# Kernel tuning notes

Measured on AMD Instinct MI355X. Metric: run time of the kernel, lower is better.

## Reference

```python
import jax, jax.numpy as jnp
import numpy as np

N_NODES = 50000
N_EDGES = 800000
IN_CH = 128
HID = 64
HEADS = 2
OUT_CH = 3
N_GRAPHS = 64
NEG_SLOPE = 0.2


def _gatv2(x, src, dst, Wl, Wr, att, bias, heads, out_ch, concat, n_nodes):
    # GATv2Conv (PyG semantics, eval mode, self-loops already appended)
    xl = (x @ Wl).reshape(n_nodes, heads, out_ch)  # lin_l -> source messages
    xr = (x @ Wr).reshape(n_nodes, heads, out_ch)  # lin_r -> target side
    e = jax.nn.leaky_relu(xl[src] + xr[dst], NEG_SLOPE)          # [E, H, C]
    alpha = jnp.einsum('ehc,hc->eh', e, att)                     # [E, H]
    # segment softmax over incoming edges of each target node
    amax = jax.ops.segment_max(alpha, dst, num_segments=n_nodes)  # [N, H]
    ea = jnp.exp(alpha - amax[dst])
    denom = jax.ops.segment_sum(ea, dst, num_segments=n_nodes)
    alpha = ea / (denom[dst] + 1e-16)
    msg = xl[src] * alpha[..., None]                             # [E, H, C]
    out = jax.ops.segment_sum(msg, dst, num_segments=n_nodes)    # [N, H, C]
    out = out.reshape(n_nodes, heads * out_ch) if concat else out.mean(axis=1)
    return out + bias


def setup_inputs() -> dict:
    key = jax.random.key(0)
    ks = jax.random.split(key, 12)
    x = jax.random.normal(ks[0], (N_NODES, IN_CH), dtype=jnp.float32)
    edge_index = jax.random.randint(ks[1], (2, N_EDGES), 0, N_NODES, dtype=jnp.int64 if jax.config.jax_enable_x64 else jnp.int32)
    batch = jnp.sort(jax.random.randint(ks[2], (N_NODES,), 0, N_GRAPHS))
    s = 0.05
    params = {
        'W1l': jax.random.normal(ks[3], (IN_CH, HEADS * HID), dtype=jnp.float32) * s,
        'W1r': jax.random.normal(ks[4], (IN_CH, HEADS * HID), dtype=jnp.float32) * s,
        'att1': jax.random.normal(ks[5], (HEADS, HID), dtype=jnp.float32) * s,
        'b1': jnp.zeros((HEADS * HID,), dtype=jnp.float32),
        'W2l': jax.random.normal(ks[6], (HEADS * HID, OUT_CH), dtype=jnp.float32) * s,
        'W2r': jax.random.normal(ks[7], (HEADS * HID, OUT_CH), dtype=jnp.float32) * s,
        'att2': jax.random.normal(ks[8], (1, OUT_CH), dtype=jnp.float32) * s,
        'b2': jnp.zeros((OUT_CH,), dtype=jnp.float32),
        'Wr1': jax.random.normal(ks[9], (OUT_CH, 64), dtype=jnp.float32) * s,
        'br1': jnp.zeros((64,), dtype=jnp.float32),
        'Wr2': jax.random.normal(ks[10], (64, 3), dtype=jnp.float32) * s,
        'br2': jnp.zeros((3,), dtype=jnp.float32),
    }
    return {'x': x, 'edge_index': edge_index, 'batch': batch, **params}


def reference(x, edge_index, batch, W1l, W1r, att1, b1, W2l, W2r, att2, b2, Wr1, br1, Wr2, br2):
    n = x.shape[0]
    loops = jnp.arange(n, dtype=edge_index.dtype)
    src = jnp.concatenate([edge_index[0], loops])  # add_self_loops=True
    dst = jnp.concatenate([edge_index[1], loops])
    h = _gatv2(x, src, dst, W1l, W1r, att1, b1, HEADS, HID, True, n)
    h = jax.nn.elu(h)
    h = _gatv2(h, src, dst, W2l, W2r, att2, b2, 1, OUT_CH, False, n)
    # global_mean_pool over graphs
    sums = jax.ops.segment_sum(h, batch, num_segments=N_GRAPHS)
    cnt = jax.ops.segment_sum(jnp.ones((n,), h.dtype), batch, num_segments=N_GRAPHS)
    g = sums / jnp.maximum(cnt, 1.0)[:, None]
    g = jax.nn.relu(g @ Wr1 + br1)
    return g @ Wr2 + br2
```

## Files before the change

### kernel.cpp

```cpp
#include <hip/hip_runtime.h>


#define NGRAPH 64
#define LOG2E 1.4426950408889634f

#define DPP_ROR(C, x) \
  __int_as_float(__builtin_amdgcn_update_dpp(0, __float_as_int(x), (0x120 | C), 0xF, 0xF, false))

__device__ __forceinline__ float rowsum16(float v) {
  v += DPP_ROR(8, v);
  v += DPP_ROR(4, v);
  v += DPP_ROR(2, v);
  v += DPP_ROR(1, v);
  return v;
}

__device__ __forceinline__ unsigned bf16rne(float f) {
  unsigned u = __float_as_uint(f);
  return (u + 0x7FFFu + ((u >> 16) & 1u)) >> 16;
}

__global__ void k_deg(const int* __restrict__ ei, int E, int Et,
                      int* __restrict__ deg, int* __restrict__ rank) {
  int e = blockIdx.x * blockDim.x + threadIdx.x;
  if (e >= Et) return;
  int d = (e < E) ? ei[E + e] : (e - E);
  rank[e] = atomicAdd(&deg[d], 1);
}

__global__ __launch_bounds__(256) void k_scan_part(const int* __restrict__ deg,
                                                   int* __restrict__ bsum, int n) {
  __shared__ int sd[256];
  int t = threadIdx.x;
  int i = blockIdx.x * 1024 + t * 4;
  int s = 0;
  if (i + 4 <= n) {
    int4 d = *(const int4*)&deg[i];
    s = d.x + d.y + d.z + d.w;
  } else {
    for (int j = i; j < min(i + 4, n); ++j) s += deg[j];
  }
  sd[t] = s;
  __syncthreads();
  for (int off = 128; off; off >>= 1) {
    if (t < off) sd[t] += sd[t + off];
    __syncthreads();
  }
  if (t == 0) bsum[blockIdx.x] = sd[0];
}

__global__ __launch_bounds__(64) void k_scan_top(int* __restrict__ bsum, int nb) {
  __shared__ int s[64];
  int t = threadIdx.x;
  s[t] = (t < nb) ? bsum[t] : 0;
  __syncthreads();
  int acc = 0;
  for (int j = 0; j < t; ++j) acc += s[j];
  if (t < nb) bsum[t] = acc;
}

__global__ __launch_bounds__(256) void k_scan_write(const int* __restrict__ deg,
                                                    const int* __restrict__ bsum,
                                                    int* __restrict__ row_ptr, int n) {
  __shared__ int sd[256];
  int t = threadIdx.x;
  int i = blockIdx.x * 1024 + t * 4;
  int4 d = make_int4(0, 0, 0, 0);
  bool full = (i + 4 <= n);
  if (full) d = *(const int4*)&deg[i];
  else {
    if (i + 0 < n) d.x = deg[i + 0];
    if (i + 1 < n) d.y = deg[i + 1];
    if (i + 2 < n) d.z = deg[i + 2];
    if (i + 3 < n) d.w = deg[i + 3];
  }
  int s = d.x + d.y + d.z + d.w;
  sd[t] = s;
  __syncthreads();
  for (int off = 1; off < 256; off <<= 1) {
    int v = (t >= off) ? sd[t - off] : 0;
    __syncthreads();
    sd[t] += v;
    __syncthreads();
  }
  int ex = sd[t] - s + bsum[blockIdx.x];
  int4 r;
  r.x = ex;
  r.y = ex + d.x;
  r.z = r.y + d.y;
  r.w = r.z + d.z;
  if (full) {
    *(int4*)&row_ptr[i] = r;
    if (i + 4 == n) row_ptr[n] = r.w + d.w;
  } else if (i < n) {
    int run = ex;
    int vals[4] = {d.x, d.y, d.z, d.w};
    for (int j = 0; j < 4 && i + j < n; ++j) {
      row_ptr[i + j] = run;
      run += vals[j];
    }
    if (i <= n && i + 4 > n) row_ptr[n] = run;
  }
}

__global__ void k_fill(const int* __restrict__ ei, int E, int Et,
                       const int* __restrict__ row_ptr,
                       const int* __restrict__ rank,
                       int* __restrict__ csr_src) {
  int e = blockIdx.x * blockDim.x + threadIdx.x;
  if (e >= Et) return;
  int s, d;
  if (e < E) { s = ei[e]; d = ei[E + e]; }
  else       { s = e - E; d = s; }
  csr_src[row_ptr[d] + rank[e]] = s;
}

__global__ __launch_bounds__(256) void k_gemm128(const float* __restrict__ x,
                                                 const float* __restrict__ Wl,
                                                 const float* __restrict__ Wr,
                                                 unsigned short* __restrict__ outl,
                                                 float* __restrict__ outr, int n) {
  __shared__ __align__(16) float xs[16][68];
  __shared__ __align__(16) float wsl[16][132];
  __shared__ __align__(16) float wsr[16][132];
  int t = threadIdx.x;
  int tx = t & 15, ty = t >> 4;
  int r0 = blockIdx.x * 64;
  float accl[4][8] = {};
  float accr[4][8] = {};

  int sr = t >> 2;
  int sk = (t & 3) * 4;
  int wk = t >> 5;
  int wc = (t & 31) * 4;

  for (int k0 = 0; k0 < 128; k0 += 16) {
    int gr = r0 + sr;
    float4 xv = make_float4(0.f, 0.f, 0.f, 0.f);
    if (gr < n) xv = *(const float4*)&x[(size_t)gr * 128 + k0 + sk];
    float4 wl0 = *(const float4*)&Wl[(size_t)(k0 + wk) * 128 + wc];
    float4 wl1 = *(const float4*)&Wl[(size_t)(k0 + wk + 8) * 128 + wc];
    float4 wr0 = *(const float4*)&Wr[(size_t)(k0 + wk) * 128 + wc];
    float4 wr1 = *(const float4*)&Wr[(size_t)(k0 + wk + 8) * 128 + wc];
    __syncthreads();
    xs[sk + 0][sr] = xv.x;
    xs[sk + 1][sr] = xv.y;
    xs[sk + 2][sr] = xv.z;
    xs[sk + 3][sr] = xv.w;
    *(float4*)&wsl[wk][wc] = wl0;
    *(float4*)&wsl[wk + 8][wc] = wl1;
    *(float4*)&wsr[wk][wc] = wr0;
    *(float4*)&wsr[wk + 8][wc] = wr1;
    __syncthreads();
#pragma unroll
    for (int k = 0; k < 16; ++k) {
      float4 av = *(const float4*)&xs[k][ty * 4];
      float4 bl0 = *(const float4*)&wsl[k][tx * 4];
      float4 bl1 = *(const float4*)&wsl[k][64 + tx * 4];
      float4 br0 = *(const float4*)&wsr[k][tx * 4];
      float4 br1 = *(const float4*)&wsr[k][64 + tx * 4];
      float a[4] = {av.x, av.y, av.z, av.w};
      float bl[8] = {bl0.x, bl0.y, bl0.z, bl0.w, bl1.x, bl1.y, bl1.z, bl1.w};
      float br[8] = {br0.x, br0.y, br0.z, br0.w, br1.x, br1.y, br1.z, br1.w};
#pragma unroll
      for (int i = 0; i < 4; ++i)
#pragma unroll
        for (int j = 0; j < 8; ++j) {
          accl[i][j] = fmaf(a[i], bl[j], accl[i][j]);
          accr[i][j] = fmaf(a[i], br[j], accr[i][j]);
        }
    }
  }
#pragma unroll
  for (int i = 0; i < 4; ++i) {
    int gr = r0 + ty * 4 + i;
    if (gr < n) {
      uint2 p0, p1;
      p0.x = bf16rne(accl[i][0]) | (bf16rne(accl[i][1]) << 16);
      p0.y = bf16rne(accl[i][2]) | (bf16rne(accl[i][3]) << 16);
      p1.x = bf16rne(accl[i][4]) | (bf16rne(accl[i][5]) << 16);
      p1.y = bf16rne(accl[i][6]) | (bf16rne(accl[i][7]) << 16);
      *(uint2*)&outl[(size_t)gr * 128 + tx * 4] = p0;
      *(uint2*)&outl[(size_t)gr * 128 + 64 + tx * 4] = p1;
      *(float4*)&outr[(size_t)gr * 128 + tx * 4] =
          make_float4(accr[i][0], accr[i][1], accr[i][2], accr[i][3]);
      *(float4*)&outr[(size_t)gr * 128 + 64 + tx * 4] =
          make_float4(accr[i][4], accr[i][5], accr[i][6], accr[i][7]);
    }
  }
}

__global__ __launch_bounds__(256) void k_fused1(const unsigned short* __restrict__ xl,
                                                const float* __restrict__ xr,
                                                const int* __restrict__ row_ptr,
                                                const int* __restrict__ csr_src,
                                                const float* __restrict__ att1,
                                                const float* __restrict__ b1,
                                                const float* __restrict__ W2l,
                                                const float* __restrict__ W2r,
                                                float* __restrict__ xl2,
                                                float* __restrict__ xr2, int n) {
  int wid  = (blockIdx.x * 256 + threadIdx.x) >> 6;
  int lane = threadIdx.x & 63;
  int sub  = lane & 31;
  int node = min(wid * 2 + (lane >> 5), n - 1);
  int ch = sub * 4;
  const char* xlb = (const char*)xl;
  unsigned chb = (unsigned)sub * 8u;
  float4 xrv = *(const float4*)&xr[(size_t)node * 128 + ch];
  float4 atv = *(const float4*)&att1[ch];
  atv.x *= LOG2E; atv.y *= LOG2E; atv.z *= LOG2E; atv.w *= LOG2E;
  int s0 = row_ptr[node];
  int deg = row_ptr[node + 1] - s0;
  int odeg = __shfl_xor(deg, 32);
  int mindeg = min(deg, odeg);
  int maxdeg = max(deg, odeg);
  const int* sp = csr_src + s0;

  float m = -1e30f, l = 0.f;
  float4 acc = make_float4(0.f, 0.f, 0.f, 0.f);

  float t0, t1, t2, t3;
#define UNPACK(dst, q)                                                  \
    dst.x = __uint_as_float(q.x << 16);                                 \
    dst.y = __uint_as_float(q.x & 0xFFFF0000u);                         \
    dst.z = __uint_as_float(q.y << 16);                                 \
    dst.w = __uint_as_float(q.y & 0xFFFF0000u);
#define LOGIT(p, v)                                                     \
    t0 = v.x + xrv.x; t0 = fmaxf(t0, 0.2f * t0);                        \
    t1 = v.y + xrv.y; t1 = fmaxf(t1, 0.2f * t1);                        \
    t2 = v.z + xrv.z; t2 = fmaxf(t2, 0.2f * t2);                        \
    t3 = v.w + xrv.w; t3 = fmaxf(t3, 0.2f * t3);                        \
    p = fmaf(t3, atv.w, fmaf(t2, atv.z, fmaf(t1, atv.y, t0 * atv.x)));

#define BODY(CLAMPED)                                                   \
  {                                                                     \
    int sA, sB, sC, sD;                                                 \
    if (CLAMPED) {                                                      \
      int dm1 = deg - 1;                                                \
      sA = sp[min(e + 0, dm1)];                                         \
      sB = sp[min(e + 1, dm1)];                                         \
      sC = sp[min(e + 2, dm1)];                                         \
      sD = sp[min(e + 3, dm1)];                                         \
    } else {                                                            \
      sA = sp[e + 0]; sB = sp[e + 1]; sC = sp[e + 2]; sD = sp[e + 3];   \
    }                                                                   \
    uint2 qa = *(const uint2*)(xlb + (((unsigned)sA << 8) + chb));      \
    uint2 qb = *(const uint2*)(xlb + (((unsigned)sB << 8) + chb));      \
    uint2 qc = *(const uint2*)(xlb + (((unsigned)sC << 8) + chb));      \
    uint2 qd = *(const uint2*)(xlb + (((unsigned)sD << 8) + chb));      \
    float4 xa, xb, xc, xd;                                              \
    UNPACK(xa, qa) UNPACK(xb, qb) UNPACK(xc, qc) UNPACK(xd, qd)         \
    float pa, pb, pc, pd;                                               \
    LOGIT(pa, xa) LOGIT(pb, xb) LOGIT(pc, xc) LOGIT(pd, xd)             \
    pa = rowsum16(pa);                                                  \
    pb = rowsum16(pb);                                                  \
    pc = rowsum16(pc);                                                  \
    pd = rowsum16(pd);                                                  \
    if (CLAMPED) {                                                      \
      pa = (e + 0 < deg) ? pa : -1e30f;                                 \
      pb = (e + 1 < deg) ? pb : -1e30f;                                 \
      pc = (e + 2 < deg) ? pc : -1e30f;                                 \
      pd = (e + 3 < deg) ? pd : -1e30f;                                 \
    }                                                                   \
    float mn = fmaxf(m, fmaxf(fmaxf(pa, pb), fmaxf(pc, pd)));           \
    float sc = exp2f(m - mn);                                           \
    float wa = exp2f(pa - mn);                                          \
    float wb = exp2f(pb - mn);                                          \
    float wc = exp2f(pc - mn);                                          \
    float wd = exp2f(pd - mn);                                          \
    acc.x = fmaf(wd, xd.x, fmaf(wc, xc.x, fmaf(wb, xb.x, fmaf(wa, xa.x, acc.x * sc)))); \
    acc.y = fmaf(wd, xd.y, fmaf(wc, xc.y, fmaf(wb, xb.y, fmaf(wa, xa.y, acc.y * sc)))); \
    acc.z = fmaf(wd, xd.z, fmaf(wc, xc.z, fmaf(wb, xb.z, fmaf(wa, xa.z, acc.z * sc)))); \
    acc.w = fmaf(wd, xd.w, fmaf(wc, xc.w, fmaf(wb, xb.w, fmaf(wa, xa.w, acc.w * sc)))); \
    l = fmaf(l, sc, wa + wb + wc + wd);                                 \
    m = mn;                                                             \
  }

  int e = 0;
  for (; e + 4 <= mindeg; e += 4) BODY(false)
  for (; e < maxdeg; e += 4) BODY(true)
#undef BODY
#undef LOGIT
#undef UNPACK

  float inv = 1.f / (l + 1e-16f);
  float4 b1v = *(const float4*)&b1[ch];
  float4 h;
  h.x = acc.x * inv + b1v.x; h.x = h.x > 0.f ? h.x : expm1f(h.x);
  h.y = acc.y * inv + b1v.y; h.y = h.y > 0.f ? h.y : expm1f(h.y);
  h.z = acc.z * inv + b1v.z; h.z = h.z > 0.f ? h.z : expm1f(h.z);
  h.w = acc.w * inv + b1v.w; h.w = h.w > 0.f ? h.w : expm1f(h.w);

  float4 u0 = *(const float4*)&W2l[ch * 3 + 0];
  float4 u1 = *(const float4*)&W2l[ch * 3 + 4];
  float4 u2 = *(const float4*)&W2l[ch * 3 + 8];
  float al0 = fmaf(h.w, u2.y, fmaf(h.z, u1.z, fmaf(h.y, u0.w, h.x * u0.x)));
  float al1 = fmaf(h.w, u2.z, fmaf(h.z, u1.w, fmaf(h.y, u1.x, h.x * u0.y)));
  float al2 = fmaf(h.w, u2.w, fmaf(h.z, u2.x, fmaf(h.y, u1.y, h.x * u0.z)));
  float4 v0 = *(const float4*)&W2r[ch * 3 + 0];
  float4 v1 = *(const float4*)&W2r[ch * 3 + 4];
  float4 v2 = *(const float4*)&W2r[ch * 3 + 8];
  float ar0 = fmaf(h.w, v2.y, fmaf(h.z, v1.z, fmaf(h.y, v0.w, h.x * v0.x)));
  float ar1 = fmaf(h.w, v2.z, fmaf(h.z, v1.w, fmaf(h.y, v1.x, h.x * v0.y)));
  float ar2 = fmaf(h.w, v2.w, fmaf(h.z, v2.x, fmaf(h.y, v1.y, h.x * v0.z)));
#pragma unroll
  for (int off = 1; off < 32; off <<= 1) {
    al0 += __shfl_xor(al0, off); al1 += __shfl_xor(al1, off);
    al2 += __shfl_xor(al2, off); ar0 += __shfl_xor(ar0, off);
    ar1 += __shfl_xor(ar1, off); ar2 += __shfl_xor(ar2, off);
  }
  if (sub == 0 && wid * 2 + (lane >> 5) < n) {
    *(float4*)&xl2[node * 4] = make_float4(al0, al1, al2, 0.f);
    *(float4*)&xr2[node * 4] = make_float4(ar0, ar1, ar2, 0.f);
  }
}

__global__ __launch_bounds__(256) void k_fused2(const float* __restrict__ xl2,
                                                const float* __restrict__ xr2,
                                                const int* __restrict__ row_ptr,
                                                const int* __restrict__ csr_src,
                                                const float* __restrict__ att2,
                                                const float* __restrict__ b2,
                                                const int* __restrict__ batch,
                                                float* __restrict__ gsum,
                                                float* __restrict__ gcnt, int n) {
  __shared__ float ls[NGRAPH * 3];
  __shared__ float lc[NGRAPH];
  int t = threadIdx.x;
  for (int i = t; i < NGRAPH * 3; i += 256) ls[i] = 0.f;
  for (int i = t; i < NGRAPH; i += 256) lc[i] = 0.f;
  __syncthreads();

  int node = (blockIdx.x * 256 + t) >> 4;
  int lane = t & 15;
  if (node < n) {
    float4 xrv = *(const float4*)&xr2[node * 4];
    float c0 = att2[0] * LOG2E, c1 = att2[1] * LOG2E, c2 = att2[2] * LOG2E;
    int s0 = row_ptr[node], s1 = row_ptr[node + 1];
    float m = -1e30f, l = 0.f, a0 = 0.f, a1 = 0.f, a2 = 0.f;
    for (int slot = s0 + lane; slot < s1; slot += 16) {
      int s = csr_src[slot];
      float4 xlv = *(const float4*)&xl2[s * 4];
      float t0 = xlv.x + xrv.x; t0 = fmaxf(t0, 0.2f * t0);
      float t1 = xlv.y + xrv.y; t1 = fmaxf(t1, 0.2f * t1);
      float t2 = xlv.z + xrv.z; t2 = fmaxf(t2, 0.2f * t2);
      float p = fmaf(t2, c2, fmaf(t1, c1, t0 * c0));
      float mn = fmaxf(m, p);
      float sc = exp2f(m - mn);
      float w  = exp2f(p - mn);
      a0 = a0 * sc + w * xlv.x;
      a1 = a1 * sc + w * xlv.y;
      a2 = a2 * sc + w * xlv.z;
      l = l * sc + w;
      m = mn;
    }
#define MERGE(C)                                                        \
    {                                                                   \
      float m2 = DPP_ROR(C, m);                                         \
      float l2 = DPP_ROR(C, l);                                         \
      float b0 = DPP_ROR(C, a0);                                        \
      float b1v = DPP_ROR(C, a1);                                       \
      float b2v = DPP_ROR(C, a2);                                       \
      float mn = fmaxf(m, m2);                                          \
      float sA = exp2f(m - mn);                                         \
      float sB = exp2f(m2 - mn);                                        \
      a0 = a0 * sA + b0 * sB;                                           \
      a1 = a1 * sA + b1v * sB;                                          \
      a2 = a2 * sA + b2v * sB;                                          \
      l = l * sA + l2 * sB;                                             \
      m = mn;                                                           \
    }
    MERGE(8) MERGE(4) MERGE(2) MERGE(1)
#undef MERGE
    if (lane == 0) {
      float inv = 1.f / (l + 1e-16f);
      float o0 = a0 * inv + b2[0];
      float o1 = a1 * inv + b2[1];
      float o2 = a2 * inv + b2[2];
      int b = batch[node];
      atomicAdd(&ls[b * 3 + 0], o0);
      atomicAdd(&ls[b * 3 + 1], o1);
      atomicAdd(&ls[b * 3 + 2], o2);
      atomicAdd(&lc[b], 1.f);
    }
  }
  __syncthreads();
  for (int i = t; i < NGRAPH * 3; i += 256)
    if (ls[i] != 0.f) atomicAdd(&gsum[i], ls[i]);
  for (int i = t; i < NGRAPH; i += 256)
    if (lc[i] != 0.f) atomicAdd(&gcnt[i], lc[i]);
}

__global__ __launch_bounds__(64) void k_mlp(const float* __restrict__ gsum,
                                            const float* __restrict__ gcnt,
                                            const float* __restrict__ Wr1,
                                            const float* __restrict__ br1,
                                            const float* __restrict__ Wr2,
                                            const float* __restrict__ br2,
                                            float* __restrict__ out) {
  int t = threadIdx.x;
  if (t >= NGRAPH) return;
  float cnt = fmaxf(gcnt[t], 1.f);
  float g0 = gsum[t * 3 + 0] / cnt;
  float g1 = gsum[t * 3 + 1] / cnt;
  float g2 = gsum[t * 3 + 2] / cnt;
  float o0 = br2[0], o1 = br2[1], o2 = br2[2];
  for (int j = 0; j < 64; ++j) {
    float hj = g0 * Wr1[j] + g1 * Wr1[64 + j] + g2 * Wr1[128 + j] + br1[j];
    hj = fmaxf(hj, 0.f);
    o0 = fmaf(hj, Wr2[j * 3 + 0], o0);
    o1 = fmaf(hj, Wr2[j * 3 + 1], o1);
    o2 = fmaf(hj, Wr2[j * 3 + 2], o2);
  }
  out[t * 3 + 0] = o0;
  out[t * 3 + 1] = o1;
  out[t * 3 + 2] = o2;
}

extern "C" void kernel_launch(void* const* d_in, const int* in_sizes, int n_in,
                              void* d_out, int out_size, void* d_ws, size_t ws_size,
                              hipStream_t stream) {
  const float* x    = (const float*)d_in[0];
  const int*   ei   = (const int*)d_in[1];
  const int*   batch= (const int*)d_in[2];
  const float* W1l  = (const float*)d_in[3];
  const float* W1r  = (const float*)d_in[4];
  const float* att1 = (const float*)d_in[5];
  const float* b1   = (const float*)d_in[6];
  const float* W2l  = (const float*)d_in[7];
  const float* W2r  = (const float*)d_in[8];
  const float* att2 = (const float*)d_in[9];
  const float* b2   = (const float*)d_in[10];
  const float* Wr1  = (const float*)d_in[11];
  const float* br1  = (const float*)d_in[12];
  const float* Wr2  = (const float*)d_in[13];
  const float* br2  = (const float*)d_in[14];
  float* out = (float*)d_out;

  const int N  = in_sizes[0] / 128;
  const int E  = in_sizes[1] / 2;
  const int Et = E + N;
  const int NB = (N + 1023) / 1024;

  char* p = (char*)d_ws;
  auto alloc = [&](size_t bytes) -> char* {
    char* r = p;
    p += (bytes + 255) & ~(size_t)255;
    return r;
  };
  unsigned short* xl1 = (unsigned short*)alloc((size_t)N * 128 * 2);
  float*    xr1    = (float*)alloc((size_t)N * 128 * 4);
  int*      row_ptr= (int*)alloc((size_t)(N + 1) * 4);
  int*      csr_src= (int*)alloc((size_t)Et * 4);
  int*      rank   = (int*)alloc((size_t)Et * 4);
  int*      bsum   = (int*)alloc(64 * 4);
  char*     z0     = p;
  int*      deg    = (int*)alloc((size_t)N * 4);
  float*    gsum   = (float*)alloc(NGRAPH * 3 * 4);
  float*    gcnt   = (float*)alloc(NGRAPH * 4);
  size_t    zbytes = (size_t)(p - z0);
  float*    xl2    = (float*)alloc((size_t)N * 4 * 4);
  float*    xr2    = (float*)alloc((size_t)N * 4 * 4);

  hipMemsetAsync(z0, 0, zbytes, stream);
  hipLaunchKernelGGL(k_deg, dim3((Et + 255) / 256), dim3(256), 0, stream,
                     ei, E, Et, deg, rank);
  hipLaunchKernelGGL(k_scan_part, dim3(NB), dim3(256), 0, stream, deg, bsum, N);
  hipLaunchKernelGGL(k_scan_top, dim3(1), dim3(64), 0, stream, bsum, NB);
  hipLaunchKernelGGL(k_scan_write, dim3(NB), dim3(256), 0, stream,
                     deg, bsum, row_ptr, N);
  hipLaunchKernelGGL(k_fill, dim3((Et + 255) / 256), dim3(256), 0, stream,
                     ei, E, Et, row_ptr, rank, csr_src);
  hipLaunchKernelGGL(k_gemm128, dim3((N + 63) / 64), dim3(256), 0, stream,
                     x, W1l, W1r, xl1, xr1, N);
  int waves1 = (N + 1) / 2;
  hipLaunchKernelGGL(k_fused1, dim3((waves1 * 64 + 255) / 256), dim3(256), 0, stream,
                     xl1, xr1, row_ptr, csr_src, att1, b1, W2l, W2r, xl2, xr2, N);
  hipLaunchKernelGGL(k_fused2, dim3((N * 16 + 255) / 256), dim3(256), 0, stream,
                     xl2, xr2, row_ptr, csr_src, att2, b2, batch, gsum, gcnt, N);
  hipLaunchKernelGGL(k_mlp, dim3(1), dim3(64), 0, stream,
                     gsum, gcnt, Wr1, br1, Wr2, br2, out);
}
```

Baseline: 281.8 us.

## Replace FP32 SIMT first-layer GEMM with split-bf16 MFMA GEMM

Replaces the shared-memory FP32 FMA GEMM for the first GATv2 projections with a matrix-core kernel. A new conversion kernel first splits x and the transposed weights into high and low bf16 parts. The GEMM then issues three bf16 MFMAs per tile (hi*hi, hi*lo, lo*hi) to approximate FP32 accuracy. The cost is an extra pass that writes two bf16 copies of x, an extra launch, and uncoalesced scalar output stores.

```diff
diff --git a/kernel.cpp b/kernel.cpp
--- a/kernel.cpp
+++ b/kernel.cpp
@@ -19,6 +19,9 @@
   unsigned u = __float_as_uint(f);
   return (u + 0x7FFFu + ((u >> 16) & 1u)) >> 16;
 }
+
+typedef __attribute__((ext_vector_type(8))) short bf16x8;
+typedef __attribute__((ext_vector_type(4))) float f32x4;
 
 __global__ void k_deg(const int* __restrict__ ei, int E, int Et,
                       int* __restrict__ deg, int* __restrict__ rank) {
@@ -115,78 +118,125 @@
   csr_src[row_ptr[d] + rank[e]] = s;
 }
 
-__global__ __launch_bounds__(256) void k_gemm128(const float* __restrict__ x,
-                                                 const float* __restrict__ Wl,
-                                                 const float* __restrict__ Wr,
-                                                 unsigned short* __restrict__ outl,
-                                                 float* __restrict__ outr, int n) {
-  __shared__ __align__(16) float xs[16][68];
-  __shared__ __align__(16) float wsl[16][132];
-  __shared__ __align__(16) float wsr[16][132];
-  int t = threadIdx.x;
-  int tx = t & 15, ty = t >> 4;
+__global__ __launch_bounds__(256) void k_cvt(const float* __restrict__ x,
+                                             const float* __restrict__ W1l,
+                                             const float* __restrict__ W1r,
+                                             unsigned short* __restrict__ xh,
+                                             unsigned short* __restrict__ xlo,
+                                             unsigned short* __restrict__ wh,
+                                             unsigned short* __restrict__ wlo,
+                                             int total_x, int xblk) {
+  if ((int)blockIdx.x < xblk) {
+    int i = (blockIdx.x * 256 + threadIdx.x) * 8;
+    if (i + 8 <= total_x) {
+      float4 a = *(const float4*)&x[i];
+      float4 b = *(const float4*)&x[i + 4];
+      float f[8] = {a.x, a.y, a.z, a.w, b.x, b.y, b.z, b.w};
+      unsigned hv[8], lv[8];
+#pragma unroll
+      for (int j = 0; j < 8; ++j) {
+        hv[j] = bf16rne(f[j]);
+        float r = f[j] - __uint_as_float(hv[j] << 16);
+        lv[j] = bf16rne(r);
+      }
+      uint4 ph, pl;
+      ph.x = hv[0] | (hv[1] << 16); ph.y = hv[2] | (hv[3] << 16);
+      ph.z = hv[4] | (hv[5] << 16); ph.w = hv[6] | (hv[7] << 16);
+      pl.x = lv[0] | (lv[1] << 16); pl.y = lv[2] | (lv[3] << 16);
+      pl.z = lv[4] | (lv[5] << 16); pl.w = lv[6] | (lv[7] << 16);
+      *(uint4*)&xh[i] = ph;
+      *(uint4*)&xlo[i] = pl;
+    } else {
+      for (int j = i; j < total_x; ++j) {
+        float f = x[j];
+        unsigned h = bf16rne(f);
+        xh[j] = (unsigned short)h;
+        xlo[j] = (unsigned short)bf16rne(f - __uint_as_float(h << 16));
+      }
+    }
+  } else {
+    int j = ((int)blockIdx.x - xblk) * 256 + threadIdx.x;
+    if (j < 256 * 128) {
+      int col = j >> 7, k = j & 127;
+      float w = (col < 128) ? W1l[k * 128 + col] : W1r[k * 128 + (col - 128)];
+      unsigned h = bf16rne(w);
+      wh[j] = (unsigned short)h;
+      wlo[j] = (unsigned short)bf16rne(w - __uint_as_float(h << 16));
+    }
+  }
+}
+
+__global__ __launch_bounds__(256) void k_gmfma(const unsigned short* __restrict__ xh,
+                                               const unsigned short* __restrict__ xlo,
+                                               const unsigned short* __restrict__ wh,
+                                               const unsigned short* __restrict__ wlo,
+                                               unsigned short* __restrict__ outl,
+                                               float* __restrict__ outr, int n) {
+  int wid = threadIdx.x >> 6;
+  int lane = threadIdx.x & 63;
+  int lr = lane & 15;
+  int lk = (lane >> 4) * 8;
   int r0 = blockIdx.x * 64;
-  float accl[4][8] = {};
-  float accr[4][8] = {};
-
-  int sr = t >> 2;
-  int sk = (t & 3) * 4;
-  int wk = t >> 5;
-  int wc = (t & 31) * 4;
-
-  for (int k0 = 0; k0 < 128; k0 += 16) {
-    int gr = r0 + sr;
-    float4 xv = make_float4(0.f, 0.f, 0.f, 0.f);
-    if (gr < n) xv = *(const float4*)&x[(size_t)gr * 128 + k0 + sk];
-    float4 wl0 = *(const float4*)&Wl[(size_t)(k0 + wk) * 128 + wc];
-    float4 wl1 = *(const float4*)&Wl[(size_t)(k0 + wk + 8) * 128 + wc];
-    float4 wr0 = *(const float4*)&Wr[(size_t)(k0 + wk) * 128 + wc];
-    float4 wr1 = *(const float4*)&Wr[(size_t)(k0 + wk + 8) * 128 + wc];
-    __syncthreads();
-    xs[sk + 0][sr] = xv.x;
-    xs[sk + 1][sr] = xv.y;
-    xs[sk + 2][sr] = xv.z;
-    xs[sk + 3][sr] = xv.w;
-    *(float4*)&wsl[wk][wc] = wl0;
-    *(float4*)&wsl[wk + 8][wc] = wl1;
-    *(float4*)&wsr[wk][wc] = wr0;
-    *(float4*)&wsr[wk + 8][wc] = wr1;
-    __syncthreads();
-#pragma unroll
-    for (int k = 0; k < 16; ++k) {
-      float4 av = *(const float4*)&xs[k][ty * 4];
-      float4 bl0 = *(const float4*)&wsl[k][tx * 4];
-      float4 bl1 = *(const float4*)&wsl[k][64 + tx * 4];
-      float4 br0 = *(const float4*)&wsr[k][tx * 4];
-      float4 br1 = *(const float4*)&wsr[k][64 + tx * 4];
-      float a[4] = {av.x, av.y, av.z, av.w};
-      float bl[8] = {bl0.x, bl0.y, bl0.z, bl0.w, bl1.x, bl1.y, bl1.z, bl1.w};
-      float br[8] = {br0.x, br0.y, br0.z, br0.w, br1.x, br1.y, br1.z, br1.w};
-#pragma unroll
-      for (int i = 0; i < 4; ++i)
-#pragma unroll
-        for (int j = 0; j < 8; ++j) {
-          accl[i][j] = fmaf(a[i], bl[j], accl[i][j]);
-          accr[i][j] = fmaf(a[i], br[j], accr[i][j]);
+  int wcol = wid * 64;
+
+  int rows[4];
+#pragma unroll
+  for (int m = 0; m < 4; ++m) rows[m] = min(r0 + m * 16 + lr, n - 1);
+
+  f32x4 acc[4][4] = {};
+
+#pragma unroll
+  for (int kc = 0; kc < 4; ++kc) {
+    int ko = kc * 32 + lk;
+    bf16x8 ah[4], al[4], bh[4], bl[4];
+#pragma unroll
+    for (int m = 0; m < 4; ++m) {
+      ah[m] = *(const bf16x8*)&xh[(size_t)rows[m] * 128 + ko];
+      al[m] = *(const bf16x8*)&xlo[(size_t)rows[m] * 128 + ko];
+    }
+#pragma unroll
+    for (int f = 0; f < 4; ++f) {
+      int c = wcol + f * 16 + lr;
+      bh[f] = *(const bf16x8*)&wh[c * 128 + ko];
+      bl[f] = *(const bf16x8*)&wlo[c * 128 + ko];
+    }
+#pragma unroll
+    for (int m = 0; m < 4; ++m)
+#pragma unroll
+      for (int f = 0; f < 4; ++f) {
+        acc[m][f] = __builtin_amdgcn_mfma_f32_16x16x32_bf16(ah[m], bh[f], acc[m][f], 0, 0, 0);
+        acc[m][f] = __builtin_amdgcn_mfma_f32_16x16x32_bf16(ah[m], bl[f], acc[m][f], 0, 0, 0);
+        acc[m][f] = __builtin_amdgcn_mfma_f32_16x16x32_bf16(al[m], bh[f], acc[m][f], 0, 0, 0);
+      }
+  }
+
+  int rbase = (lane >> 4) * 4;
+  if (wid < 2) {
+#pragma unroll
+    for (int m = 0; m < 4; ++m)
+#pragma unroll
+      for (int f = 0; f < 4; ++f) {
+        int col = wcol + f * 16 + lr;
+#pragma unroll
+        for (int i = 0; i < 4; ++i) {
+          int row = r0 + m * 16 + rbase + i;
+          if (row < n)
+            outl[(size_t)row * 128 + col] = (unsigned short)bf16rne(acc[m][f][i]);
         }
-    }
-  }
-#pragma unroll
-  for (int i = 0; i < 4; ++i) {
-    int gr = r0 + ty * 4 + i;
-    if (gr < n) {
-      uint2 p0, p1;
-      p0.x = bf16rne(accl[i][0]) | (bf16rne(accl[i][1]) << 16);
-      p0.y = bf16rne(accl[i][2]) | (bf16rne(accl[i][3]) << 16);
-      p1.x = bf16rne(accl[i][4]) | (bf16rne(accl[i][5]) << 16);
-      p1.y = bf16rne(accl[i][6]) | (bf16rne(accl[i][7]) << 16);
-      *(uint2*)&outl[(size_t)gr * 128 + tx * 4] = p0;
-      *(uint2*)&outl[(size_t)gr * 128 + 64 + tx * 4] = p1;
-      *(float4*)&outr[(size_t)gr * 128 + tx * 4] =
-          make_float4(accr[i][0], accr[i][1], accr[i][2], accr[i][3]);
-      *(float4*)&outr[(size_t)gr * 128 + 64 + tx * 4] =
-          make_float4(accr[i][4], accr[i][5], accr[i][6], accr[i][7]);
-    }
+      }
+  } else {
+#pragma unroll
+    for (int m = 0; m < 4; ++m)
+#pragma unroll
+      for (int f = 0; f < 4; ++f) {
+        int col = (wid - 2) * 64 + f * 16 + lr;
+#pragma unroll
+        for (int i = 0; i < 4; ++i) {
+          int row = r0 + m * 16 + rbase + i;
+          if (row < n)
+            outr[(size_t)row * 128 + col] = acc[m][f][i];
+        }
+      }
   }
 }
 
@@ -462,6 +512,10 @@
   size_t    zbytes = (size_t)(p - z0);
   float*    xl2    = (float*)alloc((size_t)N * 4 * 4);
   float*    xr2    = (float*)alloc((size_t)N * 4 * 4);
+  unsigned short* xh  = (unsigned short*)alloc((size_t)N * 128 * 2);
+  unsigned short* xlo = (unsigned short*)alloc((size_t)N * 128 * 2);
+  unsigned short* wth = (unsigned short*)alloc((size_t)256 * 128 * 2);
+  unsigned short* wtl = (unsigned short*)alloc((size_t)256 * 128 * 2);
 
   hipMemsetAsync(z0, 0, zbytes, stream);
   hipLaunchKernelGGL(k_deg, dim3((Et + 255) / 256), dim3(256), 0, stream,
@@ -472,8 +526,13 @@
                      deg, bsum, row_ptr, N);
   hipLaunchKernelGGL(k_fill, dim3((Et + 255) / 256), dim3(256), 0, stream,
                      ei, E, Et, row_ptr, rank, csr_src);
-  hipLaunchKernelGGL(k_gemm128, dim3((N + 63) / 64), dim3(256), 0, stream,
-                     x, W1l, W1r, xl1, xr1, N);
+  const int total_x = N * 128;
+  const int xblk = (total_x + 2047) / 2048;
+  const int wblk = (256 * 128 + 255) / 256;
+  hipLaunchKernelGGL(k_cvt, dim3(xblk + wblk), dim3(256), 0, stream,
+                     x, W1l, W1r, xh, xlo, wth, wtl, total_x, xblk);
+  hipLaunchKernelGGL(k_gmfma, dim3((N + 63) / 64), dim3(256), 0, stream,
+                     xh, xlo, wth, wtl, xl1, xr1, N);
   int waves1 = (N + 1) / 2;
   hipLaunchKernelGGL(k_fused1, dim3((waves1 * 64 + 255) / 256), dim3(256), 0, stream,
                      xl1, xr1, row_ptr, csr_src, att1, b1, W2l, W2r, xl2, xr2, N);
```

Result: no change. 277.5 us (-1.5%).
